# Kernel optimization log

Hardware: AMD Instinct MI355X
Metric: run time of the kernel (lower is better)

The kernel has to match this reference:

```python
import jax, jax.numpy as jnp
import numpy as np

B, T, D = 2, 2048, 4096
H, KVH = 32, 8            # query heads, kv heads (GQA)
HD = D // H               # 128
N_REP = H // KVH          # 4
ROPE_THETA = 500000.0


def _rope_freqs(seq_len, head_dim, theta):
    inv = 1.0 / (theta ** (np.arange(0, head_dim, 2, dtype=np.float32) / head_dim))
    ang = np.outer(np.arange(seq_len, dtype=np.float32), inv)  # [T, HD/2]
    return jnp.asarray(np.cos(ang)), jnp.asarray(np.sin(ang))


def setup_inputs() -> dict:
    key = jax.random.key(0)
    ks = jax.random.split(key, 5)
    scale = 1.0 / np.sqrt(D)
    x = jax.random.normal(ks[0], (B, T, D), dtype=jnp.float32) * 0.05
    wq = jax.random.normal(ks[1], (H * HD, D), dtype=jnp.float32) * scale
    wk = jax.random.normal(ks[2], (KVH * HD, D), dtype=jnp.float32) * scale
    wv = jax.random.normal(ks[3], (KVH * HD, D), dtype=jnp.float32) * scale
    wo = jax.random.normal(ks[4], (D, H * HD), dtype=jnp.float32) * scale
    fc, fs = _rope_freqs(T, HD, ROPE_THETA)
    return {"x": x, "wq": wq, "wk": wk, "wv": wv, "wo": wo,
            "freqs_cos": fc, "freqs_sin": fs, "start_pos": 0}


def _apply_rope(t, cos, sin):
    # t: [B, T, h, HD]; cos/sin: [T, HD/2] -> broadcast [1, T, 1, HD/2]
    b, s, h, hd = t.shape
    tr = t.reshape(b, s, h, hd // 2, 2)
    te, to = tr[..., 0], tr[..., 1]
    c = cos[None, :, None, :]
    s_ = sin[None, :, None, :]
    out = jnp.stack([te * c - to * s_, te * s_ + to * c], axis=-1)
    return out.reshape(b, s, h, hd)


def reference(x, wq, wk, wv, wo, freqs_cos, freqs_sin, start_pos):
    # Projections (F.linear convention: y = x @ W.T)
    q = jnp.einsum('btd,od->bto', x, wq).reshape(B, T, H, HD)
    k = jnp.einsum('btd,od->bto', x, wk).reshape(B, T, KVH, HD)
    v = jnp.einsum('btd,od->bto', x, wv).reshape(B, T, KVH, HD)
    # RoPE on q and k
    q = _apply_rope(q, freqs_cos, freqs_sin)
    k = _apply_rope(k, freqs_cos, freqs_sin)
    # prefill at start_pos=0: cache[:T] == k, v; repeat kv heads for GQA
    keys = jnp.repeat(k, N_REP, axis=2)    # [B, T, H, HD]
    values = jnp.repeat(v, N_REP, axis=2)  # [B, T, H, HD]
    scale = 1.0 / jnp.sqrt(jnp.float32(HD))
    # NOTE: the source module accepts a mask but never applies it -> unmasked softmax
    scores = jnp.einsum('bthd,bshd->bhts', q, keys) * scale  # [B, H, T, T]
    probs = jax.nn.softmax(scores, axis=-1)
    ctx = jnp.einsum('bhts,bshd->bthd', probs, values)       # [B, T, H, HD]
    ctx = ctx.reshape(B, T, H * HD)
    return jnp.einsum('bte,oe->bto', ctx, wo)
```

## Files before the change

### kernel.cpp

```cpp
#include <hip/hip_runtime.h>

#define B_ 2
#define T_ 2048
#define D_ 4096
#define H_ 32
#define KVH_ 8
#define HD_ 128

typedef float f32x4 __attribute__((ext_vector_type(4)));
typedef unsigned int u32x4 __attribute__((ext_vector_type(4)));
typedef unsigned short u16x4 __attribute__((ext_vector_type(4)));
typedef __bf16 bf16x8 __attribute__((ext_vector_type(8)));

__device__ __forceinline__ unsigned short f2bf(float f) {
  union { float f; unsigned int u; } x; x.f = f;
  unsigned int r = x.u + 0x7fffu + ((x.u >> 16) & 1u);
  return (unsigned short)(r >> 16);
}

__device__ __forceinline__ bf16x8 ldb8(const unsigned short* p) {
  return __builtin_bit_cast(bf16x8, *(const u32x4*)p);
}

__device__ __forceinline__ f32x4 mfma16(bf16x8 a, bf16x8 b, f32x4 c) {
  return __builtin_amdgcn_mfma_f32_16x16x32_bf16(a, b, c, 0, 0, 0);
}

__device__ __forceinline__ void gl_lds16(const void* g, void* l) {
  __builtin_amdgcn_global_load_lds(
      (const __attribute__((address_space(1))) unsigned int*)g,
      (__attribute__((address_space(3))) unsigned int*)l, 16, 0, 0);
}

__global__ __launch_bounds__(256) void cast_bf16(const float* __restrict__ src,
                                                 unsigned short* __restrict__ dst, int n4) {
  int i = blockIdx.x * 256 + threadIdx.x;
  if (i >= n4) return;
  f32x4 v = *(const f32x4*)(src + (size_t)i * 4);
  u16x4 o; o.x = f2bf(v.x); o.y = f2bf(v.y); o.z = f2bf(v.z); o.w = f2bf(v.w);
  *(u16x4*)(dst + (size_t)i * 4) = o;
}

template <int EPI>
__global__ __launch_bounds__(512, 2) void gemm_bt(const unsigned short* __restrict__ A,
                                                  const unsigned short* __restrict__ Bt,
                                                  float* __restrict__ Cf,
                                                  unsigned short* __restrict__ Qb,
                                                  unsigned short* __restrict__ Kb,
                                                  unsigned short* __restrict__ vb,
                                                  const float* __restrict__ fc,
                                                  const float* __restrict__ fs, int N) {
  const int nwg = gridDim.x * gridDim.y;
  const int orig = blockIdx.y * gridDim.x + blockIdx.x;
  const int cpx = nwg >> 3;
  const int swz = (orig & 7) * cpx + (orig >> 3);
  const int m0 = (swz / gridDim.x) * 256;
  const int n0 = (swz % gridDim.x) * 256;

  const int tid = threadIdx.x, lane = tid & 63, wave = tid >> 6;
  const int quad = lane >> 4, l16 = lane & 15;
  const int wm = wave >> 2, wn = wave & 3;
  const int sw2 = (l16 >> 1) & 3;
  const int cp = (quad ^ sw2) * 8;

  __shared__ unsigned short As[3][256 * 32];
  __shared__ unsigned short Bs[3][256 * 32];

  f32x4 acc[8][4];
#pragma unroll
  for (int i = 0; i < 8; ++i)
#pragma unroll
    for (int j = 0; j < 4; ++j) { f32x4 z = {0.f, 0.f, 0.f, 0.f}; acc[i][j] = z; }

  auto stageA = [&](int slot, int kk, int p) {
    int c = p * 512 + tid;
    int row = c >> 2, gc = (c & 3) ^ ((row >> 1) & 3);
    gl_lds16(&A[(size_t)(m0 + row) * 4096 + kk + gc * 8], &As[slot][c * 8]);
  };
  auto stageB = [&](int slot, int kk, int p) {
    int c = p * 512 + tid;
    int row = c >> 2, gc = (c & 3) ^ ((row >> 1) & 3);
    gl_lds16(&Bt[(size_t)(n0 + row) * 4096 + kk + gc * 8], &Bs[slot][c * 8]);
  };

#pragma unroll
  for (int p = 0; p < 2; ++p) stageA(0, 0, p);
#pragma unroll
  for (int p = 0; p < 2; ++p) stageB(0, 0, p);
#pragma unroll
  for (int p = 0; p < 2; ++p) stageA(1, 32, p);
#pragma unroll
  for (int p = 0; p < 2; ++p) stageB(1, 32, p);
  asm volatile("s_waitcnt vmcnt(4)" ::: "memory");
  __builtin_amdgcn_sched_barrier(0);
  __builtin_amdgcn_s_barrier();

  const int NT = 4096 / 32;
  int slot = 0, nslot = 2;

#pragma unroll 1
  for (int t = 0; t < NT; ++t) {
    const bool stage_on = (t < NT - 2);
    const int kk2 = (t + 2) * 32;
    const unsigned short* Asl = As[slot];
    const unsigned short* Bsl = Bs[slot];

    bf16x8 bfr[4], af[8];
#pragma unroll
    for (int ni = 0; ni < 4; ++ni)
      bfr[ni] = ldb8(&Bsl[(wn * 64 + ni * 16 + l16) * 32 + cp]);
#pragma unroll
    for (int mi = 0; mi < 8; ++mi)
      af[mi] = ldb8(&Asl[(wm * 128 + mi * 16 + l16) * 32 + cp]);
    if (stage_on) {
      stageA(nslot, kk2, 0); stageA(nslot, kk2, 1);
      stageB(nslot, kk2, 0); stageB(nslot, kk2, 1);
    }
    __builtin_amdgcn_s_setprio(1);
#pragma unroll
    for (int mi = 0; mi < 8; ++mi)
#pragma unroll
      for (int ni = 0; ni < 4; ++ni)
        acc[mi][ni] = mfma16(af[mi], bfr[ni], acc[mi][ni]);
    __builtin_amdgcn_s_setprio(0);
    __builtin_amdgcn_sched_barrier(0);
    if (t < NT - 1) {
      if (stage_on) {
        asm volatile("s_waitcnt vmcnt(4)" ::: "memory");
      } else {
        asm volatile("s_waitcnt vmcnt(0)" ::: "memory");
      }
      __builtin_amdgcn_sched_barrier(0);
      __builtin_amdgcn_s_barrier();
    }
    slot = (slot == 2) ? 0 : slot + 1;
    nslot = (nslot == 2) ? 0 : nslot + 1;
  }

#pragma unroll
  for (int mt = 0; mt < 8; ++mt)
#pragma unroll
    for (int nt = 0; nt < 4; ++nt)
#pragma unroll
      for (int r = 0; r < 4; ++r) {
        int m = m0 + wm * 128 + mt * 16 + quad * 4 + r;
        int n = n0 + wn * 64 + nt * 16 + l16;
        float v = acc[mt][nt][r];
        if constexpr (EPI == 0) {
          Cf[(size_t)m * N + n] = v;
        } else {
          int b = m >> 11, t = m & 2047;
          if (n0 < 4096) {
            int hh = n >> 7, hd = n & 127;
            float p = __shfl_xor(v, 1);
            int fi = t * 64 + (hd >> 1);
            float c = fc[fi], s = fs[fi];
            float o = (hd & 1) ? (p * s + v * c) : (v * c - p * s);
            o *= 0.08838834764831845f;
            Qb[((size_t)(b * H_ + hh) * T_ + t) * HD_ + hd] = f2bf(o);
          } else if (n0 < 5120) {
            int nk = n - 4096;
            int hh = nk >> 7, hd = nk & 127;
            float p = __shfl_xor(v, 1);
            int fi = t * 64 + (hd >> 1);
            float c = fc[fi], s = fs[fi];
            float o = (hd & 1) ? (p * s + v * c) : (v * c - p * s);
            Kb[((size_t)(b * KVH_ + hh) * T_ + t) * HD_ + hd] = f2bf(o);
          } else {
            vb[(size_t)m * 1024 + (n - 5120)] = f2bf(v);
          }
        }
      }
}

__global__ __launch_bounds__(256) void transpose_v(const unsigned short* __restrict__ vb,
                                                   unsigned short* __restrict__ vt) {
  __shared__ unsigned short tile[64 * 72];
  const int hd0 = blockIdx.x * 64;
  const int t0 = blockIdx.y * 64;
  const int bk = blockIdx.z;
  const int b = bk >> 3, kvh = bk & 7;
  const int tid = threadIdx.x;
#pragma unroll
  for (int p = 0; p < 2; ++p) {
    int idx = tid + p * 256;
    int tl = idx >> 3, c8 = (idx & 7) << 3;
    u16x4 lo = *(const u16x4*)&vb[((size_t)(b * T_ + t0 + tl) * KVH_ + kvh) * HD_ + hd0 + c8];
    u16x4 hi = *(const u16x4*)&vb[((size_t)(b * T_ + t0 + tl) * KVH_ + kvh) * HD_ + hd0 + c8 + 4];
#pragma unroll
    for (int j = 0; j < 4; ++j) { tile[(c8 + j) * 72 + tl] = lo[j]; tile[(c8 + 4 + j) * 72 + tl] = hi[j]; }
  }
  __syncthreads();
#pragma unroll
  for (int p = 0; p < 2; ++p) {
    int idx = tid + p * 256;
    int hdl = idx >> 3, c8 = (idx & 7) << 3;
    *(u32x4*)&vt[((size_t)(bk * HD_ + hd0 + hdl)) * T_ + t0 + c8] = *(const u32x4*)&tile[hdl * 72 + c8];
  }
}

__global__ __launch_bounds__(256, 3) void attn(const unsigned short* __restrict__ Q,
                                               const unsigned short* __restrict__ K,
                                               const unsigned short* __restrict__ Vt,
                                               unsigned short* __restrict__ ctx) {
  const int qb = blockIdx.x;
  const int bh = blockIdx.y;
  const int b = bh >> 5, h = bh & 31;
  const int kvh = h >> 2;
  const unsigned short* Qh = Q + (size_t)(b * H_ + h) * T_ * HD_;
  const unsigned short* Kh = K + (size_t)(b * KVH_ + kvh) * T_ * HD_;
  const unsigned short* Vh = Vt + (size_t)(b * KVH_ + kvh) * HD_ * T_;
  const int tid = threadIdx.x, lane = tid & 63, wave = tid >> 6;
  const int quad = lane >> 4, l16 = lane & 15;
  const int sw = l16 & 7;
  __shared__ unsigned short Ks[64 * 128];
  __shared__ unsigned short Vs[128 * 64];
  __shared__ unsigned short Ps[4][32 * 72];

  const int q0 = qb * 128 + wave * 32;
  bf16x8 qf[2][4];
#pragma unroll
  for (int mt = 0; mt < 2; ++mt)
#pragma unroll
    for (int ks = 0; ks < 4; ++ks)
      qf[mt][ks] = ldb8(&Qh[(size_t)(q0 + mt * 16 + l16) * HD_ + ks * 32 + quad * 8]);

  f32x4 o[2][8];
#pragma unroll
  for (int mt = 0; mt < 2; ++mt)
#pragma unroll
    for (int f = 0; f < 8; ++f) { f32x4 z = {0.f, 0.f, 0.f, 0.f}; o[mt][f] = z; }
  float l_part[2][4] = {{0.f, 0.f, 0.f, 0.f}, {0.f, 0.f, 0.f, 0.f}};

  for (int kb = 0; kb < T_ / 64; ++kb) {
#pragma unroll
    for (int p = 0; p < 4; ++p) {
      int c = p * 256 + tid;
      int row = c >> 4, gc = (c & 15) ^ (row & 7);
      gl_lds16(&Kh[(size_t)(kb * 64 + row) * HD_ + gc * 8], &Ks[c * 8]);
    }
#pragma unroll
    for (int p = 0; p < 4; ++p) {
      int c = p * 256 + tid;
      int row = c >> 3, gc = (c & 7) ^ (row & 7);
      gl_lds16(&Vh[(size_t)row * T_ + kb * 64 + gc * 8], &Vs[c * 8]);
    }
    __syncthreads();

    f32x4 s[2][4];
#pragma unroll
    for (int mt = 0; mt < 2; ++mt)
#pragma unroll
      for (int nt = 0; nt < 4; ++nt) { f32x4 z = {0.f, 0.f, 0.f, 0.f}; s[mt][nt] = z; }
    __builtin_amdgcn_s_setprio(1);
#pragma unroll
    for (int ks = 0; ks < 4; ++ks) {
      const int cp = ((ks * 4 + quad) ^ sw) * 8;
#pragma unroll
      for (int nt = 0; nt < 4; ++nt) {
        bf16x8 kf = ldb8(&Ks[(nt * 16 + l16) * 128 + cp]);
        s[0][nt] = mfma16(qf[0][ks], kf, s[0][nt]);
        s[1][nt] = mfma16(qf[1][ks], kf, s[1][nt]);
      }
    }
    __builtin_amdgcn_s_setprio(0);

#pragma unroll
    for (int mt = 0; mt < 2; ++mt)
#pragma unroll
      for (int nt = 0; nt < 4; ++nt)
#pragma unroll
        for (int r = 0; r < 4; ++r) {
          float p_ = __expf(s[mt][nt][r]);
          l_part[mt][r] += p_;
          Ps[wave][(mt * 16 + quad * 4 + r) * 72 + nt * 16 + l16] = f2bf(p_);
        }

    __builtin_amdgcn_s_setprio(1);
#pragma unroll
    for (int ks2 = 0; ks2 < 2; ++ks2) {
      const int cp = ((ks2 * 4 + quad) ^ sw) * 8;
      bf16x8 pf0 = ldb8(&Ps[wave][(l16) * 72 + ks2 * 32 + quad * 8]);
      bf16x8 pf1 = ldb8(&Ps[wave][(16 + l16) * 72 + ks2 * 32 + quad * 8]);
#pragma unroll
      for (int f = 0; f < 8; ++f) {
        bf16x8 vfr = ldb8(&Vs[(f * 16 + l16) * 64 + cp]);
        o[0][f] = mfma16(pf0, vfr, o[0][f]);
        o[1][f] = mfma16(pf1, vfr, o[1][f]);
      }
    }
    __builtin_amdgcn_s_setprio(0);
    __syncthreads();
  }

  float rl[2][4];
#pragma unroll
  for (int mt = 0; mt < 2; ++mt)
#pragma unroll
    for (int r = 0; r < 4; ++r) {
      float l = l_part[mt][r];
      l += __shfl_xor(l, 1);
      l += __shfl_xor(l, 2);
      l += __shfl_xor(l, 4);
      l += __shfl_xor(l, 8);
      rl[mt][r] = 1.0f / l;
    }

#pragma unroll
  for (int mt = 0; mt < 2; ++mt)
#pragma unroll
    for (int f = 0; f < 8; ++f)
#pragma unroll
      for (int r = 0; r < 4; ++r) {
        int t = qb * 128 + wave * 32 + mt * 16 + quad * 4 + r;
        int hd = f * 16 + l16;
        ctx[((size_t)(b * T_ + t)) * D_ + h * HD_ + hd] = f2bf(o[mt][f][r] * rl[mt][r]);
      }
}

extern "C" void kernel_launch(void* const* d_in, const int* in_sizes, int n_in,
                              void* d_out, int out_size, void* d_ws, size_t ws_size,
                              hipStream_t stream) {
  const float* x  = (const float*)d_in[0];
  const float* wq = (const float*)d_in[1];
  const float* wk = (const float*)d_in[2];
  const float* wv = (const float*)d_in[3];
  const float* wo = (const float*)d_in[4];
  const float* fc = (const float*)d_in[5];
  const float* fs = (const float*)d_in[6];

  char* ws = (char*)d_ws;
  unsigned short* xb   = (unsigned short*)(ws + 0);
  unsigned short* wqkv = (unsigned short*)(ws + 33554432);
  unsigned short* wob  = (unsigned short*)(ws + 83886080);
  unsigned short* ctxb = (unsigned short*)(ws + 117440512);
  unsigned short* vb   = (unsigned short*)(ws + 134217728);
  unsigned short* Qb   = (unsigned short*)(ws + 150994944);
  unsigned short* Kb   = (unsigned short*)(ws + 184549376);
  unsigned short* Vtb  = (unsigned short*)(ws + 192937984);
  float* out = (float*)d_out;

  cast_bf16<<<16384, 256, 0, stream>>>(x,  xb,  4194304);
  cast_bf16<<<16384, 256, 0, stream>>>(wq, wqkv,                       4194304);
  cast_bf16<<<4096,  256, 0, stream>>>(wk, wqkv + (size_t)4096 * 4096, 1048576);
  cast_bf16<<<4096,  256, 0, stream>>>(wv, wqkv + (size_t)5120 * 4096, 1048576);
  cast_bf16<<<16384, 256, 0, stream>>>(wo, wob, 4194304);

  gemm_bt<1><<<dim3(24, 16), 512, 0, stream>>>(xb, wqkv, nullptr, Qb, Kb, vb, fc, fs, 6144);

  transpose_v<<<dim3(2, 32, 16), 256, 0, stream>>>(vb, Vtb);

  attn<<<dim3(16, 64), 256, 0, stream>>>(Qb, Kb, Vtb, ctxb);

  gemm_bt<0><<<dim3(16, 16), 512, 0, stream>>>(ctxb, wob, out, nullptr, nullptr, nullptr, fc, fs, 4096);
}
```

Measured before the change: 826.4 us.

## Restructure GEMM mainloop into double-buffered BK=64 with quadrant-interleaved staging

```diff
diff --git a/kernel.cpp b/kernel.cpp
--- a/kernel.cpp
+++ b/kernel.cpp
@@ -60,11 +60,10 @@
   const int tid = threadIdx.x, lane = tid & 63, wave = tid >> 6;
   const int quad = lane >> 4, l16 = lane & 15;
   const int wm = wave >> 2, wn = wave & 3;
-  const int sw2 = (l16 >> 1) & 3;
-  const int cp = (quad ^ sw2) * 8;
-
-  __shared__ unsigned short As[3][256 * 32];
-  __shared__ unsigned short Bs[3][256 * 32];
+  const int sw = l16 & 7;
+
+  __shared__ unsigned short As[2][256 * 64];
+  __shared__ unsigned short Bs[2][256 * 64];
 
   f32x4 acc[8][4];
 #pragma unroll
@@ -72,70 +71,113 @@
 #pragma unroll
     for (int j = 0; j < 4; ++j) { f32x4 z = {0.f, 0.f, 0.f, 0.f}; acc[i][j] = z; }
 
-  auto stageA = [&](int slot, int kk, int p) {
-    int c = p * 512 + tid;
-    int row = c >> 2, gc = (c & 3) ^ ((row >> 1) & 3);
-    gl_lds16(&A[(size_t)(m0 + row) * 4096 + kk + gc * 8], &As[slot][c * 8]);
-  };
-  auto stageB = [&](int slot, int kk, int p) {
-    int c = p * 512 + tid;
-    int row = c >> 2, gc = (c & 3) ^ ((row >> 1) & 3);
-    gl_lds16(&Bt[(size_t)(n0 + row) * 4096 + kk + gc * 8], &Bs[slot][c * 8]);
-  };
-
-#pragma unroll
-  for (int p = 0; p < 2; ++p) stageA(0, 0, p);
-#pragma unroll
-  for (int p = 0; p < 2; ++p) stageB(0, 0, p);
-#pragma unroll
-  for (int p = 0; p < 2; ++p) stageA(1, 32, p);
-#pragma unroll
-  for (int p = 0; p < 2; ++p) stageB(1, 32, p);
+  auto stA = [&](int d, int h, int kt) {
+#pragma unroll
+    for (int pp = 0; pp < 2; ++pp) {
+      int c = pp * 512 + tid;
+      int row = h * 128 + (c >> 3), gc = (c & 7) ^ (row & 7);
+      gl_lds16(&A[(size_t)(m0 + row) * 4096 + kt * 64 + gc * 8], &As[d][(h * 1024 + c) * 8]);
+    }
+  };
+  auto stB = [&](int d, int h, int kt) {
+#pragma unroll
+    for (int pp = 0; pp < 2; ++pp) {
+      int c = pp * 512 + tid;
+      int row = h * 128 + (c >> 3), gc = (c & 7) ^ (row & 7);
+      gl_lds16(&Bt[(size_t)(n0 + row) * 4096 + kt * 64 + gc * 8], &Bs[d][(h * 1024 + c) * 8]);
+    }
+  };
+
+  bf16x8 af[4][2], bf0[2][2], bf1[2][2];
+  auto rdA = [&](int d, int mh) {
+#pragma unroll
+    for (int mi = 0; mi < 4; ++mi)
+#pragma unroll
+      for (int ks = 0; ks < 2; ++ks)
+        af[mi][ks] = ldb8(&As[d][(wm * 128 + mh * 64 + mi * 16 + l16) * 64 + (((ks * 4 + quad)) ^ sw) * 8]);
+  };
+  auto rdB = [&](int d, int nh, bf16x8 (&bf)[2][2]) {
+#pragma unroll
+    for (int ni = 0; ni < 2; ++ni)
+#pragma unroll
+      for (int ks = 0; ks < 2; ++ks)
+        bf[ni][ks] = ldb8(&Bs[d][(wn * 64 + nh * 32 + ni * 16 + l16) * 64 + (((ks * 4 + quad)) ^ sw) * 8]);
+  };
+  auto mma = [&](int mh, int nh, bf16x8 (&bf)[2][2]) {
+    __builtin_amdgcn_s_setprio(1);
+#pragma unroll
+    for (int mi = 0; mi < 4; ++mi)
+#pragma unroll
+      for (int ni = 0; ni < 2; ++ni)
+#pragma unroll
+        for (int ks = 0; ks < 2; ++ks)
+          acc[mh * 4 + mi][nh * 2 + ni] = mfma16(af[mi][ks], bf[ni][ks], acc[mh * 4 + mi][nh * 2 + ni]);
+    __builtin_amdgcn_s_setprio(0);
+  };
+#define BAR() __builtin_amdgcn_s_barrier()
+#define LGKM0()                                          \
+  asm volatile("s_waitcnt lgkmcnt(0)" ::: "memory");     \
+  __builtin_amdgcn_sched_barrier(0)
+
+  stA(0, 0, 0); stA(0, 1, 0); stB(0, 0, 0); stB(0, 1, 0);
+  stA(1, 0, 1); stB(1, 1, 1);
   asm volatile("s_waitcnt vmcnt(4)" ::: "memory");
   __builtin_amdgcn_sched_barrier(0);
-  __builtin_amdgcn_s_barrier();
-
-  const int NT = 4096 / 32;
-  int slot = 0, nslot = 2;
-
+  BAR();
+
+  const int NJ = 4096 / 128;
 #pragma unroll 1
-  for (int t = 0; t < NT; ++t) {
-    const bool stage_on = (t < NT - 2);
-    const int kk2 = (t + 2) * 32;
-    const unsigned short* Asl = As[slot];
-    const unsigned short* Bsl = Bs[slot];
-
-    bf16x8 bfr[4], af[8];
-#pragma unroll
-    for (int ni = 0; ni < 4; ++ni)
-      bfr[ni] = ldb8(&Bsl[(wn * 64 + ni * 16 + l16) * 32 + cp]);
-#pragma unroll
-    for (int mi = 0; mi < 8; ++mi)
-      af[mi] = ldb8(&Asl[(wm * 128 + mi * 16 + l16) * 32 + cp]);
-    if (stage_on) {
-      stageA(nslot, kk2, 0); stageA(nslot, kk2, 1);
-      stageB(nslot, kk2, 0); stageB(nslot, kk2, 1);
-    }
-    __builtin_amdgcn_s_setprio(1);
-#pragma unroll
-    for (int mi = 0; mi < 8; ++mi)
-#pragma unroll
-      for (int ni = 0; ni < 4; ++ni)
-        acc[mi][ni] = mfma16(af[mi], bfr[ni], acc[mi][ni]);
-    __builtin_amdgcn_s_setprio(0);
+  for (int j = 0; j < NJ; ++j) {
+    const bool on = (j < NJ - 1);
+    const int k1 = 2 * j + 1, k2 = 2 * j + 2, k3 = 2 * j + 3;
+
+    rdA(0, 0); rdB(0, 0, bf0);
+    stA(1, 1, k1); stB(1, 0, k1);
+    BAR(); LGKM0();
+    mma(0, 0, bf0);
+    BAR();
+    rdB(0, 1, bf1);
+    BAR(); LGKM0();
+    mma(0, 1, bf1);
+    BAR();
+    rdA(0, 1);
+    if (on) stA(0, 0, k2);
+    BAR(); LGKM0();
+    mma(1, 1, bf1);
+    BAR();
+    rdB(0, 0, bf0);
+    if (on) stB(0, 1, k2);
+    BAR(); LGKM0();
+    mma(1, 0, bf0);
+    if (on) { asm volatile("s_waitcnt vmcnt(4)" ::: "memory"); }
+    else    { asm volatile("s_waitcnt vmcnt(0)" ::: "memory"); }
     __builtin_amdgcn_sched_barrier(0);
-    if (t < NT - 1) {
-      if (stage_on) {
-        asm volatile("s_waitcnt vmcnt(4)" ::: "memory");
-      } else {
-        asm volatile("s_waitcnt vmcnt(0)" ::: "memory");
-      }
-      __builtin_amdgcn_sched_barrier(0);
-      __builtin_amdgcn_s_barrier();
-    }
-    slot = (slot == 2) ? 0 : slot + 1;
-    nslot = (nslot == 2) ? 0 : nslot + 1;
+    BAR();
+    rdA(1, 0); rdB(1, 0, bf0);
+    if (on) { stA(0, 1, k2); stB(0, 0, k2); }
+    BAR(); LGKM0();
+    mma(0, 0, bf0);
+    BAR();
+    rdB(1, 1, bf1);
+    BAR(); LGKM0();
+    mma(0, 1, bf1);
+    BAR();
+    rdA(1, 1);
+    if (on) stA(1, 0, k3);
+    BAR(); LGKM0();
+    mma(1, 1, bf1);
+    BAR();
+    rdB(1, 0, bf0);
+    if (on) stB(1, 1, k3);
+    BAR(); LGKM0();
+    mma(1, 0, bf0);
+    if (on) { asm volatile("s_waitcnt vmcnt(4)" ::: "memory"); }
+    else    { asm volatile("s_waitcnt vmcnt(0)" ::: "memory"); }
+    __builtin_amdgcn_sched_barrier(0);
+    BAR();
   }
+#undef BAR
+#undef LGKM0
 
 #pragma unroll
   for (int mt = 0; mt < 8; ++mt)
```

After: 870.7 us. +5.4%, slower.

## Replace pipelined 256x256 GEMM with simple 128x128 single-buffer tiles

Applied to the files above, without the earlier changes.

```diff
diff --git a/kernel.cpp b/kernel.cpp
--- a/kernel.cpp
+++ b/kernel.cpp
@@ -42,109 +42,72 @@
 }
 
 template <int EPI>
-__global__ __launch_bounds__(512, 2) void gemm_bt(const unsigned short* __restrict__ A,
-                                                  const unsigned short* __restrict__ Bt,
-                                                  float* __restrict__ Cf,
-                                                  unsigned short* __restrict__ Qb,
-                                                  unsigned short* __restrict__ Kb,
-                                                  unsigned short* __restrict__ vb,
-                                                  const float* __restrict__ fc,
-                                                  const float* __restrict__ fs, int N) {
+__global__ __launch_bounds__(256) void gemm_bt(const unsigned short* __restrict__ A,
+                                               const unsigned short* __restrict__ Bt,
+                                               float* __restrict__ Cf,
+                                               unsigned short* __restrict__ Qb,
+                                               unsigned short* __restrict__ Kb,
+                                               unsigned short* __restrict__ vb,
+                                               const float* __restrict__ fc,
+                                               const float* __restrict__ fs, int N) {
   const int nwg = gridDim.x * gridDim.y;
   const int orig = blockIdx.y * gridDim.x + blockIdx.x;
   const int cpx = nwg >> 3;
   const int swz = (orig & 7) * cpx + (orig >> 3);
-  const int m0 = (swz / gridDim.x) * 256;
-  const int n0 = (swz % gridDim.x) * 256;
+  const int m0 = (swz / gridDim.x) * 128;
+  const int n0 = (swz % gridDim.x) * 128;
 
   const int tid = threadIdx.x, lane = tid & 63, wave = tid >> 6;
   const int quad = lane >> 4, l16 = lane & 15;
-  const int wm = wave >> 2, wn = wave & 3;
-  const int sw2 = (l16 >> 1) & 3;
-  const int cp = (quad ^ sw2) * 8;
-
-  __shared__ unsigned short As[3][256 * 32];
-  __shared__ unsigned short Bs[3][256 * 32];
-
-  f32x4 acc[8][4];
-#pragma unroll
-  for (int i = 0; i < 8; ++i)
+  const int wy = wave >> 1, wx = wave & 1;
+  const int sw = l16 & 7;
+  __shared__ unsigned short As[128 * 64];
+  __shared__ unsigned short Bs[128 * 64];
+  f32x4 acc[4][4];
+#pragma unroll
+  for (int i = 0; i < 4; ++i)
 #pragma unroll
     for (int j = 0; j < 4; ++j) { f32x4 z = {0.f, 0.f, 0.f, 0.f}; acc[i][j] = z; }
 
-  auto stageA = [&](int slot, int kk, int p) {
-    int c = p * 512 + tid;
-    int row = c >> 2, gc = (c & 3) ^ ((row >> 1) & 3);
-    gl_lds16(&A[(size_t)(m0 + row) * 4096 + kk + gc * 8], &As[slot][c * 8]);
-  };
-  auto stageB = [&](int slot, int kk, int p) {
-    int c = p * 512 + tid;
-    int row = c >> 2, gc = (c & 3) ^ ((row >> 1) & 3);
-    gl_lds16(&Bt[(size_t)(n0 + row) * 4096 + kk + gc * 8], &Bs[slot][c * 8]);
-  };
-
-#pragma unroll
-  for (int p = 0; p < 2; ++p) stageA(0, 0, p);
-#pragma unroll
-  for (int p = 0; p < 2; ++p) stageB(0, 0, p);
-#pragma unroll
-  for (int p = 0; p < 2; ++p) stageA(1, 32, p);
-#pragma unroll
-  for (int p = 0; p < 2; ++p) stageB(1, 32, p);
-  asm volatile("s_waitcnt vmcnt(4)" ::: "memory");
-  __builtin_amdgcn_sched_barrier(0);
-  __builtin_amdgcn_s_barrier();
-
-  const int NT = 4096 / 32;
-  int slot = 0, nslot = 2;
-
-#pragma unroll 1
-  for (int t = 0; t < NT; ++t) {
-    const bool stage_on = (t < NT - 2);
-    const int kk2 = (t + 2) * 32;
-    const unsigned short* Asl = As[slot];
-    const unsigned short* Bsl = Bs[slot];
-
-    bf16x8 bfr[4], af[8];
-#pragma unroll
-    for (int ni = 0; ni < 4; ++ni)
-      bfr[ni] = ldb8(&Bsl[(wn * 64 + ni * 16 + l16) * 32 + cp]);
-#pragma unroll
-    for (int mi = 0; mi < 8; ++mi)
-      af[mi] = ldb8(&Asl[(wm * 128 + mi * 16 + l16) * 32 + cp]);
-    if (stage_on) {
-      stageA(nslot, kk2, 0); stageA(nslot, kk2, 1);
-      stageB(nslot, kk2, 0); stageB(nslot, kk2, 1);
-    }
-    __builtin_amdgcn_s_setprio(1);
-#pragma unroll
-    for (int mi = 0; mi < 8; ++mi)
-#pragma unroll
-      for (int ni = 0; ni < 4; ++ni)
-        acc[mi][ni] = mfma16(af[mi], bfr[ni], acc[mi][ni]);
-    __builtin_amdgcn_s_setprio(0);
-    __builtin_amdgcn_sched_barrier(0);
-    if (t < NT - 1) {
-      if (stage_on) {
-        asm volatile("s_waitcnt vmcnt(4)" ::: "memory");
-      } else {
-        asm volatile("s_waitcnt vmcnt(0)" ::: "memory");
-      }
-      __builtin_amdgcn_sched_barrier(0);
-      __builtin_amdgcn_s_barrier();
-    }
-    slot = (slot == 2) ? 0 : slot + 1;
-    nslot = (nslot == 2) ? 0 : nslot + 1;
+  for (int k0 = 0; k0 < 4096; k0 += 64) {
+#pragma unroll
+    for (int p = 0; p < 4; ++p) {
+      int c = p * 256 + tid;
+      int row = c >> 3, gc = (c & 7) ^ (row & 7);
+      gl_lds16(&A[(size_t)(m0 + row) * 4096 + k0 + gc * 8], &As[c * 8]);
+    }
+#pragma unroll
+    for (int p = 0; p < 4; ++p) {
+      int c = p * 256 + tid;
+      int row = c >> 3, gc = (c & 7) ^ (row & 7);
+      gl_lds16(&Bt[(size_t)(n0 + row) * 4096 + k0 + gc * 8], &Bs[c * 8]);
+    }
+    __syncthreads();
+#pragma unroll
+    for (int ks = 0; ks < 2; ++ks) {
+      const int cp = ((ks * 4 + quad) ^ sw) * 8;
+      bf16x8 af[4], bfr[4];
+#pragma unroll
+      for (int mt = 0; mt < 4; ++mt) af[mt] = ldb8(&As[(wy * 64 + mt * 16 + l16) * 64 + cp]);
+#pragma unroll
+      for (int nt = 0; nt < 4; ++nt) bfr[nt] = ldb8(&Bs[(wx * 64 + nt * 16 + l16) * 64 + cp]);
+#pragma unroll
+      for (int mt = 0; mt < 4; ++mt)
+#pragma unroll
+        for (int nt = 0; nt < 4; ++nt)
+          acc[mt][nt] = mfma16(af[mt], bfr[nt], acc[mt][nt]);
+    }
+    __syncthreads();
   }
 
 #pragma unroll
-  for (int mt = 0; mt < 8; ++mt)
+  for (int mt = 0; mt < 4; ++mt)
 #pragma unroll
     for (int nt = 0; nt < 4; ++nt)
 #pragma unroll
       for (int r = 0; r < 4; ++r) {
-        int m = m0 + wm * 128 + mt * 16 + quad * 4 + r;
-        int n = n0 + wn * 64 + nt * 16 + l16;
+        int m = m0 + wy * 64 + mt * 16 + quad * 4 + r;
+        int n = n0 + wx * 64 + nt * 16 + l16;
         float v = acc[mt][nt][r];
         if constexpr (EPI == 0) {
           Cf[(size_t)m * N + n] = v;
@@ -346,11 +309,11 @@
   cast_bf16<<<4096,  256, 0, stream>>>(wv, wqkv + (size_t)5120 * 4096, 1048576);
   cast_bf16<<<16384, 256, 0, stream>>>(wo, wob, 4194304);
 
-  gemm_bt<1><<<dim3(24, 16), 512, 0, stream>>>(xb, wqkv, nullptr, Qb, Kb, vb, fc, fs, 6144);
+  gemm_bt<1><<<dim3(48, 32), 256, 0, stream>>>(xb, wqkv, nullptr, Qb, Kb, vb, fc, fs, 6144);
 
   transpose_v<<<dim3(2, 32, 16), 256, 0, stream>>>(vb, Vtb);
 
   attn<<<dim3(16, 64), 256, 0, stream>>>(Qb, Kb, Vtb, ctxb);
 
-  gemm_bt<0><<<dim3(16, 16), 512, 0, stream>>>(ctxb, wob, out, nullptr, nullptr, nullptr, fc, fs, 4096);
-}
+  gemm_bt<0><<<dim3(32, 32), 256, 0, stream>>>(ctxb, wob, out, nullptr, nullptr, nullptr, fc, fs, 4096);
+}
```

After: 923.8 us. 11.8% more time.
